# Kernel optimization log

Hardware: AMD Instinct MI355X
Metric: run time of the kernel (lower is better)

## Reference

```python
import jax, jax.numpy as jnp
import numpy as np

SIGMA = 0.02
B, CC, H, W = 4, 21, 96, 96
C_LOW, C_HIGH = 3, 512
N = H * W


def _grid_edges(h, w):
    idx = np.arange(h * w).reshape(h, w)
    eh = np.stack([idx[:, :-1].ravel(), idx[:, 1:].ravel()], 1)
    ev = np.stack([idx[:-1, :].ravel(), idx[1:, :].ravel()], 1)
    return np.concatenate([eh, ev], 0)  # [E,2] 4-connected grid edges


def _mst_bfs(feat, h, w):
    # feat: [C,h,w] numpy. Kruskal MST with norm2 edge weights, then BFS from node 0.
    n = h * w
    edges = _grid_edges(h, w)
    f = feat.reshape(feat.shape[0], -1)
    wts = ((f[:, edges[:, 0]] - f[:, edges[:, 1]]) ** 2).sum(0)
    order = np.argsort(wts, kind='stable')
    uf = np.arange(n)

    def find(x):
        r = x
        while uf[r] != r:
            r = uf[r]
        while uf[x] != r:
            uf[x], x = r, uf[x]
        return r

    adj = [[] for _ in range(n)]
    cnt = 0
    for ei in order:
        a, b = int(edges[ei, 0]), int(edges[ei, 1])
        ra, rb = find(a), find(b)
        if ra != rb:
            uf[ra] = rb
            adj[a].append(b)
            adj[b].append(a)
            cnt += 1
            if cnt == n - 1:
                break
    parent = np.zeros(n, np.int64)
    seen = np.zeros(n, bool)
    seen[0] = True
    levels, frontier = [[0]], [0]
    while frontier:
        nxt = []
        for u in frontier:
            for v in adj[u]:
                if not seen[v]:
                    seen[v] = True
                    parent[v] = u
                    nxt.append(v)
        if nxt:
            levels.append(nxt)
        frontier = nxt
    return parent, levels


def _tree_arrays(embed):
    # Host-side MST + BFS level schedule (integer tree topology, non-differentiable).
    e = np.asarray(jax.device_get(embed)).astype(np.float64)
    bn = e.shape[0]
    parents, levels = [], []
    for b in range(bn):
        p, lv = _mst_bfs(e[b], H, W)
        parents.append(p)
        levels.append(lv)
    D = max(len(lv) for lv in levels)
    L = max(max(len(l) for l in lv) for lv in levels)
    nodes = np.full((bn, D, L), N, np.int32)  # index N = dummy sink node
    for b, lv in enumerate(levels):
        for d, l in enumerate(lv):
            nodes[b, d, :len(l)] = l
    par = np.stack(parents)
    par = np.concatenate([par, np.full((bn, 1), N)], 1).astype(np.int32)
    msk = np.ones((bn, N + 1), np.float32)
    msk[:, 0] = 0.0  # root has no parent edge
    msk[:, N] = 0.0  # dummy node
    return jnp.asarray(nodes), jnp.asarray(par), jnp.asarray(msk)


def _tree_filter(feat, embed, nodes, parent, wmask, sigma):
    # feat [B,C,N], embed [B,Ce,N]. O(N) two-pass (leaf->root, root->leaf) tree DP:
    # out_i = sum_j (prod_{e in path(i,j)} w_e) f_j / same-with-f=1
    bn, c, nn = feat.shape
    ez = jnp.pad(embed, ((0, 0), (0, 0), (0, 1)))  # add dummy column
    ep = jax.vmap(lambda e, p: e[:, p])(ez, parent)  # parent embedding [B,Ce,N+1]
    w = wmask * jnp.exp(-((ez - ep) ** 2).sum(1) / sigma)  # edge weight per node [B,N+1]
    fa = jnp.concatenate([feat, jnp.ones((bn, 1, nn), feat.dtype)], 1)  # append norm channel
    fa = jnp.pad(fa, ((0, 0), (0, 0), (0, 1)))  # [B,C+1,N+1]

    def one(a0, wv, par, lvls):
        def up(a, lvl):  # children before parents: subtree aggregation
            return a.at[:, par[lvl]].add(wv[lvl] * a[:, lvl]), None
        a, _ = jax.lax.scan(up, a0, lvls[::-1])

        def down(s, lvl):  # parents before children: whole-tree aggregation
            wl = wv[lvl]
            sv = a[:, lvl] + wl * (s[:, par[lvl]] - wl * a[:, lvl])
            return s.at[:, lvl].set(sv), None
        s, _ = jax.lax.scan(down, a, lvls)
        return s

    s = jax.vmap(one)(fa, w, parent, nodes)
    return s[:, :c, :nn] / s[:, c:, :nn]


def _nearest(x, h, w):
    hr, wr = x.shape[-2:]
    ri = jnp.arange(h) * hr // h
    ci = jnp.arange(w) * wr // w
    return x[..., ri[:, None], ci[None, :]]


def setup_inputs():
    key = jax.random.key(0)
    k1, k2, k3, k4 = jax.random.split(key, 4)
    preds = jax.random.normal(k1, (B, CC, H, W), jnp.float32)
    low_feats = jax.random.uniform(k2, (B, C_LOW, H, W), dtype=jnp.float32)
    high_feats = 0.03 * jax.random.normal(k3, (B, C_HIGH, H, W), jnp.float32)
    roi = (jax.random.uniform(k4, (B, 1, 2 * H, 2 * W)) > 0.5).astype(jnp.float32)
    return {'preds': preds, 'low_feats': low_feats, 'high_feats': high_feats,
            'unlabeled_ROIs': roi}


def reference(preds, low_feats, high_feats, unlabeled_ROIs):
    nodes_l, par_l, msk_l = _tree_arrays(low_feats)
    nodes_h, par_h, msk_h = _tree_arrays(high_feats)
    roi = _nearest(unlabeled_ROIs, H, W)
    n = roi.sum()
    prob = jax.nn.sigmoid(preds)
    lf = low_feats.reshape(B, C_LOW, N)
    hf = high_feats.reshape(B, C_HIGH, N)
    AS = _tree_filter(prob.reshape(B, CC, N), lf, nodes_l, par_l, msk_l, SIGMA)
    AS = _tree_filter(AS, hf, nodes_h, par_h, msk_h, 1.0)
    loss = (roi * jnp.abs(prob - AS.reshape(B, CC, H, W))).sum()
    return jnp.where(n > 0, loss / n, jnp.zeros_like(loss))
```

## Files before the change

kernel.cpp:

```cpp
#include <hip/hip_runtime.h>
#include <math.h>
#include <stdint.h>
#include <stddef.h>


namespace {
constexpr int Bn  = 4, Cc = 21, Hh = 96, Ww = 96;
constexpr int Nn  = Hh * Ww;
constexpr int EhE = Hh * (Ww - 1);
constexpr int Ne  = EhE + (Hh - 1) * Ww;
constexpr int Clow = 3, Chigh = 512;
constexpr int NCh = Cc + 1;
constexpr int MAXD = 2048;
constexpr int TL  = 2 * (Nn - 1);
constexpr int ESL = 18432;
constexpr int SEG = 19;
constexpr int NR  = (TL + SEG - 1) / SEG;
constexpr int MAXC = 4608;

constexpr size_t OFF_ACC  = 0;
constexpr size_t OFF_PROB = 256;
constexpr size_t OFF_S1   = OFF_PROB + (size_t)Bn * Cc * Nn * 4;
constexpr size_t OFF_S2   = OFF_S1   + (size_t)Bn * NCh * Nn * 4;
constexpr size_t OFF_EW   = OFF_S2   + (size_t)Bn * NCh * Nn * 4;
constexpr size_t OFF_ORD  = OFF_EW   + (size_t)8 * Ne * 8;
constexpr size_t OFF_PPOS = OFF_ORD  + (size_t)8 * Nn * 4;
constexpr size_t OFF_WGT  = OFF_PPOS + (size_t)8 * Nn * 2;
constexpr size_t OFF_LEV  = OFF_WGT  + (size_t)8 * Nn * 4;
constexpr size_t OFF_D    = OFF_LEV  + (size_t)8 * MAXD * 4;
constexpr size_t OFF_DIR  = OFF_D    + 256;
constexpr size_t OFF_CBW  = OFF_DIR  + (size_t)8 * Nn * 4;
constexpr size_t OFF_CBE  = OFF_CBW  + (size_t)8 * Nn * 8;
constexpr size_t OFF_OPP  = OFF_CBE  + (size_t)8 * Nn * 4;
constexpr size_t OFF_SGN  = OFF_OPP  + (size_t)8 * ESL * 2;
constexpr size_t OFF_PNF  = OFF_SGN  + (size_t)8 * ESL;
constexpr size_t OFF_RNK  = OFF_PNF  + (size_t)8 * Nn * 4;
constexpr size_t OFF_PAIR = OFF_RNK  + (size_t)8 * ESL * 2;
constexpr size_t OFF_EL1  = OFF_ORD;
constexpr size_t OFF_EL2  = OFF_WGT;
}

__device__ __forceinline__ void edge_nodes(int e, int& a, int& b) {
    if (e < EhE) { int h = e / (Ww - 1), w = e - h * (Ww - 1); a = h * Ww + w; b = a + 1; }
    else { int e2 = e - EhE; int h = e2 / Ww, w = e2 - h * Ww; a = h * Ww + w; b = a + Ww; }
}
__device__ __forceinline__ int dir_delta(int d) {
    return (d == 0) ? 1 : (d == 1) ? -1 : (d == 2) ? Ww : -Ww;
}
__device__ __forceinline__ int edge_of(int u, int d) {
    int h = u / Ww, w = u - h * Ww;
    if (d == 0) return h * (Ww - 1) + w;
    if (d == 1) return h * (Ww - 1) + w - 1;
    if (d == 2) return EhE + u;
    return EhE + u - Ww;
}

__device__ __forceinline__ unsigned long long mkkey(double w, int e) {
    unsigned long long q = (unsigned long long)(w * 70368744177664.0);
    if (q >= (1ull << 49)) q = (1ull << 49) - 1;
    return (q << 15) | (unsigned)e;
}

__device__ __forceinline__ void compact_push(bool keep, int val, int* cnt,
                                             unsigned short* out, int lane) {
    unsigned long long m = __ballot(keep ? 1 : 0);
    if (m == 0ull) return;
    int leader = __ffsll((unsigned long long)m) - 1;
    int base = 0;
    if (lane == leader) base = atomicAdd(cnt, __popcll(m));
    base = __shfl(base, leader, 64);
    if (keep) {
        unsigned long long lower = m & ((1ull << lane) - 1ull);
        out[base + __popcll(lower)] = (unsigned short)val;
    }
}

__device__ __forceinline__ int scan1024s(int val, int tid, int* wsum) {
    __syncthreads();
    int lane = tid & 63, wv = tid >> 6;
    int x = val;
    #pragma unroll
    for (int off = 1; off < 64; off <<= 1) {
        int y = __shfl_up(x, off, 64);
        if (lane >= off) x += y;
    }
    if (lane == 63) wsum[wv] = x;
    __syncthreads();
    if (wv == 0) {
        int s2 = (lane < 16) ? wsum[lane] : 0;
        #pragma unroll
        for (int off = 1; off < 16; off <<= 1) {
            int y = __shfl_up(s2, off, 64);
            if (lane >= off) s2 += y;
        }
        if (lane < 16) wsum[lane] = s2;
    }
    __syncthreads();
    int base = (wv > 0) ? wsum[wv - 1] : 0;
    return x + base;
}

__device__ __forceinline__ int scan1024_incl(int val, int tid, int* b0, int* b1) {
    b0[tid] = val;
    __syncthreads();
    int* s = b0; int* d = b1;
    for (int off = 1; off < 1024; off <<= 1) {
        int x = s[tid];
        if (tid >= off) x += s[tid - off];
        d[tid] = x;
        __syncthreads();
        int* t = s; s = d; d = t;
    }
    return s[tid];
}

__global__ void k_init(const float* __restrict__ preds, float* __restrict__ prob,
                       double* __restrict__ acc) {
    int idx = blockIdx.x * blockDim.x + threadIdx.x;
    if (idx == 0) { acc[0] = 0.0; acc[1] = 0.0; }
    if (idx >= Bn * Cc * Nn) return;
    prob[idx] = 1.0f / (1.0f + expf(-preds[idx]));
}

__global__ void k_edgew(const float* __restrict__ feat, int C, double* __restrict__ ew) {
    int idx = blockIdx.x * blockDim.x + threadIdx.x;
    if (idx >= Bn * Ne) return;
    int b = idx / Ne, e = idx - b * Ne;
    int a, c2; edge_nodes(e, a, c2);
    const float* fa = feat + (size_t)b * C * Nn + a;
    const float* fb = feat + (size_t)b * C * Nn + c2;
    double s = 0.0;
    int c = 0;
    for (; c + 16 <= C; c += 16) {
        float va[16], vb[16];
        #pragma unroll
        for (int k = 0; k < 16; k++) {
            va[k] = fa[(size_t)(c + k) * Nn];
            vb[k] = fb[(size_t)(c + k) * Nn];
        }
        #pragma unroll
        for (int k = 0; k < 16; k++) {
            double d = (double)va[k] - (double)vb[k];
            s += d * d;
        }
    }
    for (; c < C; c++) {
        double d = (double)fa[(size_t)c * Nn] - (double)fb[(size_t)c * Nn];
        s += d * d;
    }
    ew[idx] = s;
}

__global__ void __launch_bounds__(1024)
k_mst(char* __restrict__ ws) {
    const int tb = blockIdx.x, tid = threadIdx.x;
    const int lane = tid & 63;
    const double* ew = (const double*)(ws + OFF_EW) + (size_t)tb * Ne;
    int* dirG = (int*)(ws + OFF_DIR) + (size_t)tb * Nn;
    unsigned short* elA = (unsigned short*)(ws + OFF_EL1) + (size_t)tb * Ne;
    unsigned short* elB = (unsigned short*)(ws + OFF_EL2) + (size_t)tb * Ne;

    __shared__ unsigned short comp[Nn];
    __shared__ unsigned long long cbK[MAXC];
    __shared__ int scanBuf[2048];
    __shared__ int chgArr[48];
    __shared__ int sLen, sNC;

    unsigned short* nxtN     = (unsigned short*)cbK;
    unsigned short* newSlotN = (unsigned short*)cbK + Nn;
    unsigned short* nxt      = (unsigned short*)cbK;
    unsigned short* newSlot  = (unsigned short*)cbK + MAXC;

    for (int i = tid; i < Nn; i += 1024) dirG[i] = 0;
    if (tid < 48) chgArr[tid] = 0;
    __syncthreads();

    for (int i = tid; i < Nn; i += 1024) {
        int h = i / Ww, w = i - h * Ww;
        unsigned long long bk = ~0ull;
        if (w < Ww - 1) { int e = h * (Ww - 1) + w;     unsigned long long k = mkkey(ew[e], e); if (k < bk) bk = k; }
        if (w > 0)      { int e = h * (Ww - 1) + w - 1; unsigned long long k = mkkey(ew[e], e); if (k < bk) bk = k; }
        if (h < Hh - 1) { int e = EhE + i;              unsigned long long k = mkkey(ew[e], e); if (k < bk) bk = k; }
        if (h > 0)      { int e = EhE + i - Ww;         unsigned long long k = mkkey(ew[e], e); if (k < bk) bk = k; }
        int e = (int)(bk & 0x7FFF);
        int a, c; edge_nodes(e, a, c);
        nxtN[i] = (unsigned short)((a == i) ? c : a);
        int da = (c == a + 1) ? 0 : 2;
        atomicOr(&dirG[a], 1 << da);
        atomicOr(&dirG[c], 1 << (da ^ 1));
    }
    __syncthreads();
    for (int i = tid; i < Nn; i += 1024) {
        int o = nxtN[i];
        if (o != i && nxtN[o] == i && i < o) nxtN[i] = (unsigned short)i;
    }
    __syncthreads();
    {
        int it = 0;
        while (it < 40) {
            bool any = false;
            for (int r = tid; r < Nn; r += 1024) {
                int nr = nxtN[r], nnr = nxtN[nr];
                if (nr != nnr) { nxtN[r] = (unsigned short)nnr; any = true; }
            }
            if (any) chgArr[it] = 1;
            __syncthreads();
            if (!chgArr[it]) break;
            it++;
        }
    }
    {
        int base = tid * 9, cnt = 0, loc[9];
        #pragma unroll
        for (int k = 0; k < 9; k++) {
            int i = base + k;
            loc[k] = cnt;
            if (nxtN[i] == i) cnt++;
        }
        int incl = scan1024_incl(cnt, tid, scanBuf, scanBuf + 1024);
        int eb = incl - cnt;
        #pragma unroll
        for (int k = 0; k < 9; k++) {
            int i = base + k;
            if (nxtN[i] == i) newSlotN[i] = (unsigned short)(eb + loc[k]);
        }
        if (tid == 1023) sNC = incl;
    }
    __syncthreads();
    for (int i = tid; i < Nn; i += 1024) comp[i] = newSlotN[nxtN[i]];
    __syncthreads();
    int nComp = sNC;

    unsigned short* src = elA;
    unsigned short* dst = elB;
    int srcLen = -1;
    for (int round = 2; round < 22 && nComp > 1; round++) {
        if (tid == 0) sLen = 0;
        if (tid < 48) chgArr[tid] = 0;
        __syncthreads();
        if (srcLen < 0) {
            for (int e = tid; e < Ne; e += 1024) {
                int a, c; edge_nodes(e, a, c);
                compact_push(comp[a] != comp[c], e, &sLen, dst, lane);
            }
        } else {
            for (int k = tid; k < srcLen; k += 1024) {
                int e = src[k];
                int a, c; edge_nodes(e, a, c);
                compact_push(comp[a] != comp[c], e, &sLen, dst, lane);
            }
        }
        for (int s = tid; s < nComp; s += 1024) cbK[s] = ~0ull;
        __syncthreads();
        int len = sLen;
        if (len == 0) break;
        for (int k = tid; k < len; k += 1024) {
            int e = dst[k];
            int a, c; edge_nodes(e, a, c);
            unsigned long long key = mkkey(ew[e], e);
            atomicMin(&cbK[comp[a]], key);
            atomicMin(&cbK[comp[c]], key);
        }
        __syncthreads();
        unsigned long long kr[5];
        int nOwn = 0;
        for (int s = tid; s < nComp; s += 1024) kr[nOwn++] = cbK[s];
        __syncthreads();
        {
            int o = 0;
            for (int s = tid; s < nComp; s += 1024, o++) {
                unsigned long long key = kr[o];
                if (key != ~0ull) {
                    int e = (int)(key & 0x7FFF);
                    int a, c; edge_nodes(e, a, c);
                    int sa = comp[a], sc = comp[c];
                    nxt[s] = (unsigned short)((sa == s) ? sc : sa);
                    int da = (c == a + 1) ? 0 : 2;
                    atomicOr(&dirG[a], 1 << da);
                    atomicOr(&dirG[c], 1 << (da ^ 1));
                } else nxt[s] = (unsigned short)s;
            }
        }
        __syncthreads();
        for (int s = tid; s < nComp; s += 1024) {
            int o = nxt[s];
            if (o != s && nxt[o] == s && s < o) nxt[s] = (unsigned short)s;
        }
        __syncthreads();
        {
            int it = 0;
            while (it < 40) {
                bool any = false;
                for (int s = tid; s < nComp; s += 1024) {
                    int ns = nxt[s], nns = nxt[ns];
                    if (ns != nns) { nxt[s] = (unsigned short)nns; any = true; }
                }
                if (any) chgArr[it] = 1;
                __syncthreads();
                if (!chgArr[it]) break;
                it++;
            }
        }
        {
            int K = (nComp + 1023) >> 10;
            int base = tid * K, cnt = 0, loc[5];
            for (int k = 0; k < K; k++) {
                int s = base + k;
                loc[k] = cnt;
                if (s < nComp && nxt[s] == s) cnt++;
            }
            int incl = scan1024_incl(cnt, tid, scanBuf, scanBuf + 1024);
            int eb = incl - cnt;
            for (int k = 0; k < K; k++) {
                int s = base + k;
                if (s < nComp && nxt[s] == s) newSlot[s] = (unsigned short)(eb + loc[k]);
            }
            if (tid == 1023) sNC = incl;
        }
        __syncthreads();
        for (int i = tid; i < Nn; i += 1024) comp[i] = newSlot[nxt[comp[i]]];
        __syncthreads();
        nComp = sNC;
        unsigned short* t = src; src = dst; dst = t;
        srcLen = len;
    }
}

__global__ void __launch_bounds__(1024)
k_topo(char* __restrict__ ws) {
    const int tb = blockIdx.x, tid = threadIdx.x;
    const int lane = tid & 63, wv = tid >> 6;
    const int tree = tb >> 2;
    const double* ew  = (const double*)(ws + OFF_EW) + (size_t)tb * Ne;
    const int*  dirG  = (const int*)(ws + OFF_DIR) + (size_t)tb * Nn;
    unsigned int*   elemSegG = (unsigned int*)(ws + OFF_CBW + (size_t)tb * 73728);
    unsigned short* ORG      = (unsigned short*)(ws + OFF_CBW + (size_t)tb * 73728);
    unsigned short* OWNR     = ORG + ESL;
    unsigned short* ownG     = (unsigned short*)(ws + OFF_CBE + (size_t)tb * (size_t)ESL * 2);
    unsigned short* oppG     = (unsigned short*)(ws + OFF_OPP + (size_t)tb * (size_t)ESL * 2);
    unsigned short* IRG      = (unsigned short*)(ws + OFF_SGN + (size_t)tb * ESL);
    unsigned short* rank0G   = (unsigned short*)(ws + OFF_RNK + (size_t)tb * (size_t)ESL * 2);
    int*            ordG  = (int*)(ws + OFF_ORD)  + (size_t)tb * Nn;
    uint2*          pairG = (uint2*)(ws + OFF_PAIR) + (size_t)tb * Nn;
    int*            levG  = (int*)(ws + OFF_LEV)  + (size_t)tb * MAXD;
    int*            dG    = (int*)(ws + OFF_D);
    const float inv_sigma = tree ? 1.0f : 50.0f;

    __shared__ char A[36864];
    __shared__ char B[18432];
    __shared__ char C[9216];
    __shared__ int  wsum[16];
    __shared__ int  sR, sPack, sCenter;

    unsigned short* degOff = (unsigned short*)B;
    unsigned char*  nbS    = (unsigned char*)C;
    for (int i = tid; i < Nn; i += 1024) nbS[i] = (unsigned char)dirG[i];
    __syncthreads();
    {
        int base9 = tid * 9;
        int loc[9]; int s = 0;
        #pragma unroll
        for (int k = 0; k < 9; k++) { loc[k] = s; s += __popc(nbS[base9 + k]); }
        int incl = scan1024s(s, tid, wsum);
        int eb = incl - s;
        #pragma unroll
        for (int k = 0; k < 9; k++) degOff[base9 + k] = (unsigned short)(eb + loc[k]);
    }
    __syncthreads();

    unsigned short* nxtS = (unsigned short*)A;
    for (int u = tid; u < Nn; u += 1024) {
        int m = nbS[u]; int base = degOff[u]; int k = 0;
        #pragma unroll
        for (int d = 0; d < 4; d++) {
            if (m & (1 << d)) {
                int v = u + dir_delta(d);
                int mv = nbS[v]; int rd = d ^ 1;
                int pv = __popc(mv & ((1 << rd) - 1));
                int dv = __popc(mv);
                int nx = pv + 1; if (nx == dv) nx = 0;
                int j = base + k;
                nxtS[j] = (unsigned short)(degOff[v] + nx);
                ownG[j] = (unsigned short)((u << 2) | d);
                oppG[j] = (unsigned short)(degOff[v] + pv);
                k++;
            }
        }
    }
    __syncthreads();

    int myNr = 0, myLen = 0;
    if (tid < NR) {
        int x = tid * SEG, off = 0;
        for (int g = 0; g < 4096; g++) {
            elemSegG[x] = ((unsigned)tid << 11) | (unsigned)off;
            int y = nxtS[x];
            if (y % SEG == 0) { myNr = y / SEG; myLen = off + 1; break; }
            x = y; off++;
        }
    }
    __syncthreads();

    unsigned short* cn  = (unsigned short*)C;
    unsigned short* cd  = (unsigned short*)(C + 2048);
    unsigned short* nn2 = (unsigned short*)(C + 4096);
    unsigned short* nd2 = (unsigned short*)(C + 6144);
    if (tid == 0)      { cn[0] = 0; cd[0] = 0; }
    else if (tid < NR) { cn[tid] = (unsigned short)myNr; cd[tid] = (unsigned short)myLen; }
    else               { cn[tid] = (unsigned short)tid; cd[tid] = 0; }
    __syncthreads();
    for (int r = 0; r < 10; r++) {
        int c = cn[tid];
        int dv = cd[tid] + cd[c];
        int n2 = cn[c];
        nn2[tid] = (unsigned short)n2; nd2[tid] = (unsigned short)dv;
        __syncthreads();
        unsigned short* t;
        t = cn; cn = nn2; nn2 = t;
        t = cd; cd = nd2; nd2 = t;
    }
    unsigned short* rb = nn2;
    rb[tid] = (tid == 0) ? 0 : (unsigned short)(TL - cd[tid]);
    __syncthreads();

    for (int hh = 0; hh < 2; hh++) {
        unsigned int pk4[9];
        #pragma unroll
        for (int t = 0; t < 9; t++) {
            int e = tid + (hh * 9 + t) * 1024;
            pk4[t] = elemSegG[e < TL ? e : 0];
        }
        unsigned short rbv[9];
        #pragma unroll
        for (int t = 0; t < 9; t++) rbv[t] = rb[pk4[t] >> 11];
        #pragma unroll
        for (int t = 0; t < 9; t++) {
            int e = tid + (hh * 9 + t) * 1024;
            if (e < TL) rank0G[e] = (unsigned short)(rbv[t] + (pk4[t] & 2047));
        }
    }
    __syncthreads();

    for (int hh = 0; hh < 2; hh++) {
        unsigned short rnk[9], opp[9], own2[9];
        #pragma unroll
        for (int t = 0; t < 9; t++) {
            int j = tid + (hh * 9 + t) * 1024;
            int ja = j < TL ? j : 0;
            rnk[t] = rank0G[ja]; opp[t] = oppG[ja]; own2[t] = ownG[ja];
        }
        unsigned short r2[9];
        #pragma unroll
        for (int t = 0; t < 9; t++) r2[t] = rank0G[opp[t]];
        #pragma unroll
        for (int t = 0; t < 9; t++) {
            int j = tid + (hh * 9 + t) * 1024;
            if (j < TL) { int r = rnk[t]; ORG[r] = r2[t]; OWNR[r] = own2[t]; }
        }
    }
    {
        unsigned short dof[9];
        #pragma unroll
        for (int t = 0; t < 9; t++) dof[t] = degOff[tid + t * 1024];
        unsigned short ov[9];
        #pragma unroll
        for (int t = 0; t < 9; t++) ov[t] = oppG[dof[t]];
        unsigned short rv[9];
        #pragma unroll
        for (int t = 0; t < 9; t++) rv[t] = rank0G[ov[t]];
        #pragma unroll
        for (int t = 0; t < 9; t++) IRG[tid + t * 1024] = rv[t];
    }
    __syncthreads();

    short* scanS = (short*)A;
    unsigned char* parC = (unsigned char*)C;
    unsigned short* depthB = (unsigned short*)B;
    int curRoot = 0, rootC = 0;
    for (int ph = 0; ph < 3; ph++) {
        if (tid == 0) {
            sR = ORG[IRG[curRoot]];
            sPack = 0;
        }
        __syncthreads();
        const int R = sR;
        const bool doPar = (ph >= 1);
        int base = tid * 18;
        int n = TL - base; if (n > 18) n = 18; if (n < 0) n = 0;
        unsigned short orvA[18], ownA[18];
        #pragma unroll
        for (int k = 0; k < 18; k++) {
            int q = base + k;
            int r = q + R; if (r >= TL) r -= TL; if (q >= TL) r = 0;
            orvA[k] = ORG[r];
        }
        if (doPar) {
            #pragma unroll
            for (int k = 0; k < 18; k++) {
                int q = base + k;
                int r = q + R; if (r >= TL) r -= TL; if (q >= TL) r = 0;
                ownA[k] = OWNR[r];
            }
        }
        short loc[18]; int s = 0;
        #pragma unroll
        for (int k = 0; k < 18; k++) {
            if (k < n) {
                int q = base + k;
                int rro = (int)orvA[k] - R; if (rro < 0) rro += TL;
                bool desc = q < rro;
                if (doPar && desc) {
                    int own = ownA[k];
                    int head = (own >> 2) + dir_delta(own & 3);
                    parC[head] = (unsigned char)((own & 3) ^ 1);
                }
                s += desc ? 1 : -1;
                loc[k] = (short)s;
            }
        }
        int incl = scan1024s(s, tid, wsum);
        int eb = incl - s;
        #pragma unroll
        for (int k = 0; k < 18; k++)
            if (k < n) scanS[base + k] = (short)(loc[k] + eb);
        __syncthreads();
        int pk = 0;
        {
            unsigned short qA[9];
            #pragma unroll
            for (int j = 0; j < 9; j++) qA[j] = IRG[tid + j * 1024];
            int depA[9];
            #pragma unroll
            for (int j = 0; j < 9; j++) {
                int q = (int)qA[j] - R; if (q < 0) q += TL;
                depA[j] = (int)scanS[q];
            }
            #pragma unroll
            for (int j = 0; j < 9; j++) {
                int x = tid + j * 1024;
                int dep = (x == curRoot) ? 0 : depA[j];
                int p2 = (dep << 14) | x;
                if (p2 > pk) pk = p2;
                if (ph == 2) depthB[x] = (unsigned short)dep;
            }
        }
        #pragma unroll
        for (int off = 32; off > 0; off >>= 1) {
            int o = __shfl_down(pk, off, 64);
            if (o > pk) pk = o;
        }
        if (lane == 0) atomicMax(&sPack, pk);
        __syncthreads();
        if (ph == 0) curRoot = sPack & 16383;
        else if (ph == 1) {
            int diam = sPack >> 14, v = sPack & 16383;
            int steps = diam - (diam >> 1);
            unsigned short* J  = (unsigned short*)A;
            unsigned short* J2 = (unsigned short*)(A + 18432);
            for (int x = tid; x < Nn; x += 1024)
                J[x] = (unsigned short)((x == curRoot) ? x : (x + dir_delta(parC[x])));
            if (tid == 0) sCenter = v;
            __syncthreads();
            for (int k = 0; (steps >> k) != 0; k++) {
                if (tid == 0 && ((steps >> k) & 1)) sCenter = J[sCenter];
                if ((steps >> (k + 1)) != 0) {
                    __syncthreads();
                    for (int x = tid; x < Nn; x += 1024) J2[x] = J[J[x]];
                    __syncthreads();
                    unsigned short* t = J; J = J2; J2 = t;
                }
            }
            __syncthreads();
            curRoot = sCenter;
            rootC = curRoot;
        }
        __syncthreads();
    }
    const int D = (sPack >> 14) + 1;

    unsigned short* posOf = (unsigned short*)A;
    int* hist   = (int*)(A + 18432);
    int* levOff = (int*)(A + 26624);
    for (int k = tid; k < 2048; k += 1024) hist[k] = 0;
    __syncthreads();
    for (int v = tid; v < Nn; v += 1024) atomicAdd(&hist[depthB[v]], 1);
    __syncthreads();
    {
        int h0 = hist[2 * tid], h1 = hist[2 * tid + 1];
        int partial = h0 + h1;
        int incl = scan1024s(partial, tid, wsum);
        int eb = incl - partial;
        levOff[2 * tid] = eb;
        levOff[2 * tid + 1] = eb + h0;
    }
    __syncthreads();
    for (int d = tid; d <= D && d < 2048; d += 1024) levG[d] = levOff[d];
    for (int k = tid; k < 2048; k += 1024) hist[k] = 0;
    __syncthreads();
    for (int v = tid; v < Nn; v += 1024) {
        int dep = depthB[v];
        int pos = levOff[dep] + atomicAdd(&hist[dep], 1);
        posOf[v] = (unsigned short)pos;
        ordG[pos] = v;
    }
    __syncthreads();

    {
        unsigned char rdA[9]; unsigned short posA[9];
        #pragma unroll
        for (int t = 0; t < 9; t++) {
            int v = tid + t * 1024;
            rdA[t] = parC[v]; posA[t] = posOf[v];
        }
        double ewv[9]; unsigned short ppv[9];
        #pragma unroll
        for (int t = 0; t < 9; t++) {
            int v = tid + t * 1024;
            int rd = rdA[t] & 3;
            bool ir = (v == rootC);
            int p  = ir ? v : v + dir_delta(rd);
            int ei = ir ? 0 : edge_of(v, rd);
            ppv[t] = posOf[p];
            ewv[t] = ew[ei];
        }
        #pragma unroll
        for (int t = 0; t < 9; t++) {
            int v = tid + t * 1024;
            int pos = posA[t];
            if (v == rootC) {
                pairG[pos] = make_uint2(0u, 0u);
            } else {
                float w = expf(-(float)ewv[t] * inv_sigma);
                pairG[pos] = make_uint2(__float_as_uint(w), (unsigned)ppv[t]);
            }
        }
    }
    if (tid == 0) dG[tb] = D;
}

__global__ void __launch_bounds__(64)
k_dp(char* __restrict__ ws, int tree, int inMode) {
    const int bc = blockIdx.x;
    const int b = bc / NCh, c = bc % NCh;
    const int tb = tree * Bn + b;
    const int lane = threadIdx.x;
    const int*   ordG  = (const int*)(ws + OFF_ORD)  + (size_t)tb * Nn;
    const uint2* pairG = (const uint2*)(ws + OFF_PAIR) + (size_t)tb * Nn;
    const int*   levG  = (const int*)(ws + OFF_LEV)  + (size_t)tb * MAXD;
    const int D = ((const int*)(ws + OFF_D))[tb];
    const float* src = (inMode == 0)
        ? (const float*)(ws + OFF_PROB) + ((size_t)b * Cc + c) * Nn
        : (const float*)(ws + OFF_S1)   + ((size_t)b * NCh + c) * Nn;
    const float* srcN = (const float*)(ws + OFF_S1) + ((size_t)b * NCh + Cc) * Nn;
    float* dst = (float*)(ws + (tree ? OFF_S2 : OFF_S1)) + ((size_t)b * NCh + c) * Nn;

    __shared__ alignas(16) float Al[Nn];
    __shared__ alignas(16) uint2 pairS[Nn];
    __shared__ unsigned short levS[MAXD];

    {
        const uint4* pg4 = (const uint4*)pairG;
        uint4* ps4 = (uint4*)pairS;
        for (int k = lane; k < Nn / 2; k += 64) ps4[k] = pg4[k];
    }
    for (int d = lane; d <= D && d < MAXD; d += 64) levS[d] = (unsigned short)levG[d];
    if (c == Cc)            { for (int i = lane; i < Nn; i += 64) Al[i] = 1.0f; }
    else if (inMode == 0)   { for (int i = lane; i < Nn; i += 64) Al[i] = src[ordG[i]]; }
    else                    { for (int i = lane; i < Nn; i += 64) { int nd = ordG[i]; Al[i] = src[nd] / srcN[nd]; } }
    __builtin_amdgcn_wave_barrier();
    asm volatile("" ::: "memory");

    if (D > 1) {
        int sd = levS[D - 1], sd1 = levS[D];
        for (int d = D - 1; d >= 1; d--) {
            int nbv = (d > 1) ? (int)levS[d - 1] : 0;
            for (int i = sd + lane; i < sd1; i += 64) {
                uint2 pk = pairS[i];
                atomicAdd(&Al[pk.y], __uint_as_float(pk.x) * Al[i]);
            }
            __builtin_amdgcn_wave_barrier();
            asm volatile("" ::: "memory");
            sd1 = sd; sd = nbv;
        }
    }
    if (D > 1) {
        int sd = levS[1], sd1 = levS[2];
        for (int d = 1; d < D; d++) {
            int nbv = (d + 2 <= D) ? (int)levS[d + 2] : 0;
            for (int i = sd + lane; i < sd1; i += 64) {
                uint2 pk = pairS[i];
                float w = __uint_as_float(pk.x);
                float a = Al[i];
                Al[i] = a + w * (Al[pk.y] - w * a);
            }
            __builtin_amdgcn_wave_barrier();
            asm volatile("" ::: "memory");
            sd = sd1; sd1 = nbv;
        }
    }
    __builtin_amdgcn_wave_barrier();
    asm volatile("" ::: "memory");
    for (int i = lane; i < Nn; i += 64) dst[ordG[i]] = Al[i];
}

__global__ void k_loss(char* __restrict__ ws, const float* __restrict__ roi) {
    const int tid = threadIdx.x;
    int idx = blockIdx.x * 256 + tid;
    const float* prob = (const float*)(ws + OFF_PROB);
    const float* S2   = (const float*)(ws + OFF_S2);
    double* acc = (double*)(ws + OFF_ACC);
    double ls = 0.0, cnt = 0.0;
    if (idx < Bn * Cc * Nn) {
        int b = idx / (Cc * Nn);
        int rem = idx - b * (Cc * Nn);
        int c = rem / Nn, n = rem - c * Nn;
        int h = n / Ww, w2 = n - h * Ww;
        float r = roi[(size_t)b * (2 * Hh) * (2 * Ww) + (size_t)(2 * h) * (2 * Ww) + 2 * w2];
        float as = S2[((size_t)b * NCh + c) * Nn + n] / S2[((size_t)b * NCh + Cc) * Nn + n];
        float pp = prob[((size_t)b * Cc + c) * Nn + n];
        ls = (double)(r * fabsf(pp - as));
        if (c == 0) cnt = (double)r;
    }
    __shared__ double sl[256], sc2[256];
    sl[tid] = ls; sc2[tid] = cnt;
    __syncthreads();
    for (int s = 128; s > 0; s >>= 1) {
        if (tid < s) { sl[tid] += sl[tid + s]; sc2[tid] += sc2[tid + s]; }
        __syncthreads();
    }
    if (tid == 0) { atomicAdd(acc, sl[0]); atomicAdd(acc + 1, sc2[0]); }
}

__global__ void k_final(const double* __restrict__ acc, float* __restrict__ out) {
    if (blockIdx.x == 0 && threadIdx.x == 0)
        out[0] = (acc[1] > 0.0) ? (float)(acc[0] / acc[1]) : 0.0f;
}

extern "C" void kernel_launch(void* const* d_in, const int* in_sizes, int n_in,
                              void* d_out, int out_size, void* d_ws, size_t ws_size,
                              hipStream_t stream) {
    const float* preds = (const float*)d_in[0];
    const float* lowf  = (const float*)d_in[1];
    const float* highf = (const float*)d_in[2];
    const float* roi   = (const float*)d_in[3];
    char* ws = (char*)d_ws;
    float* out = (float*)d_out;
    double* ewl = (double*)(ws + OFF_EW);
    double* ewh = (double*)(ws + OFF_EW) + (size_t)Bn * Ne;

    k_init<<<(Bn * Cc * Nn + 255) / 256, 256, 0, stream>>>(
        preds, (float*)(ws + OFF_PROB), (double*)(ws + OFF_ACC));
    k_edgew<<<(Bn * Ne + 255) / 256, 256, 0, stream>>>(lowf, Clow, ewl);
    k_edgew<<<(Bn * Ne + 255) / 256, 256, 0, stream>>>(highf, Chigh, ewh);
    k_mst<<<8, 1024, 0, stream>>>(ws);
    k_topo<<<8, 1024, 0, stream>>>(ws);
    k_dp<<<Bn * NCh, 64, 0, stream>>>(ws, 0, 0);
    k_dp<<<Bn * NCh, 64, 0, stream>>>(ws, 1, 1);
    k_loss<<<(Bn * Cc * Nn + 255) / 256, 256, 0, stream>>>(ws, roi);
    k_final<<<1, 64, 0, stream>>>((const double*)(ws + OFF_ACC), out);
}
```

Baseline: 676.7 us.

## Replace upward-pass LDS atomic scatter with child-mask gather in tree DP

After: 898.3 us. 32.8% more time.

```diff
diff --git a/kernel.cpp b/kernel.cpp
--- a/kernel.cpp
+++ b/kernel.cpp
@@ -36,6 +36,7 @@
 constexpr size_t OFF_PNF  = OFF_SGN  + (size_t)8 * ESL;
 constexpr size_t OFF_RNK  = OFF_PNF  + (size_t)8 * Nn * 4;
 constexpr size_t OFF_PAIR = OFF_RNK  + (size_t)8 * ESL * 2;
+constexpr size_t OFF_POSF = OFF_PAIR + (size_t)8 * Nn * 8;
 constexpr size_t OFF_EL1  = OFF_ORD;
 constexpr size_t OFF_EL2  = OFF_WGT;
 }
@@ -342,6 +343,7 @@
     unsigned short* rank0G   = (unsigned short*)(ws + OFF_RNK + (size_t)tb * (size_t)ESL * 2);
     int*            ordG  = (int*)(ws + OFF_ORD)  + (size_t)tb * Nn;
     uint2*          pairG = (uint2*)(ws + OFF_PAIR) + (size_t)tb * Nn;
+    unsigned short* posOfG = (unsigned short*)(ws + OFF_POSF) + (size_t)tb * Nn;
     int*            levG  = (int*)(ws + OFF_LEV)  + (size_t)tb * MAXD;
     int*            dG    = (int*)(ws + OFF_D);
     const float inv_sigma = tree ? 1.0f : 50.0f;
@@ -606,11 +608,22 @@
     __syncthreads();
 
     {
-        unsigned char rdA[9]; unsigned short posA[9];
+        unsigned char rdA[9]; unsigned short posA[9]; int mkA[9];
         #pragma unroll
         for (int t = 0; t < 9; t++) {
             int v = tid + t * 1024;
             rdA[t] = parC[v]; posA[t] = posOf[v];
+        }
+        #pragma unroll
+        for (int t = 0; t < 9; t++) {
+            int v = tid + t * 1024;
+            int h = v / Ww, w2 = v - h * Ww;
+            int mk = 0;
+            if (w2 < Ww - 1) { int u = v + 1;  if (u != rootC && parC[u] == 1) mk |= 1; }
+            if (w2 > 0)      { int u = v - 1;  if (u != rootC && parC[u] == 0) mk |= 2; }
+            if (h < Hh - 1)  { int u = v + Ww; if (u != rootC && parC[u] == 3) mk |= 4; }
+            if (h > 0)       { int u = v - Ww; if (u != rootC && parC[u] == 2) mk |= 8; }
+            mkA[t] = mk;
         }
         double ewv[9]; unsigned short ppv[9];
         #pragma unroll
@@ -627,11 +640,13 @@
         for (int t = 0; t < 9; t++) {
             int v = tid + t * 1024;
             int pos = posA[t];
+            posOfG[v] = (unsigned short)pos;
+            unsigned meta = ((unsigned)mkA[t] << 14) | ((unsigned)v << 18);
             if (v == rootC) {
-                pairG[pos] = make_uint2(0u, 0u);
+                pairG[pos] = make_uint2(0u, meta);
             } else {
                 float w = expf(-(float)ewv[t] * inv_sigma);
-                pairG[pos] = make_uint2(__float_as_uint(w), (unsigned)ppv[t]);
+                pairG[pos] = make_uint2(__float_as_uint(w), (unsigned)ppv[t] | meta);
             }
         }
     }
@@ -646,6 +661,7 @@
     const int lane = threadIdx.x;
     const int*   ordG  = (const int*)(ws + OFF_ORD)  + (size_t)tb * Nn;
     const uint2* pairG = (const uint2*)(ws + OFF_PAIR) + (size_t)tb * Nn;
+    const unsigned short* posOfG = (const unsigned short*)(ws + OFF_POSF) + (size_t)tb * Nn;
     const int*   levG  = (const int*)(ws + OFF_LEV)  + (size_t)tb * MAXD;
     const int D = ((const int*)(ws + OFF_D))[tb];
     const float* src = (inMode == 0)
@@ -656,12 +672,16 @@
 
     __shared__ alignas(16) float Al[Nn];
     __shared__ alignas(16) uint2 pairS[Nn];
+    __shared__ alignas(16) unsigned short posOfS[Nn];
     __shared__ unsigned short levS[MAXD];
 
     {
         const uint4* pg4 = (const uint4*)pairG;
         uint4* ps4 = (uint4*)pairS;
         for (int k = lane; k < Nn / 2; k += 64) ps4[k] = pg4[k];
+        const uint4* po4 = (const uint4*)posOfG;
+        uint4* pos4 = (uint4*)posOfS;
+        for (int k = lane; k < Nn / 8; k += 64) pos4[k] = po4[k];
     }
     for (int d = lane; d <= D && d < MAXD; d += 64) levS[d] = (unsigned short)levG[d];
     if (c == Cc)            { for (int i = lane; i < Nn; i += 64) Al[i] = 1.0f; }
@@ -670,13 +690,24 @@
     __builtin_amdgcn_wave_barrier();
     asm volatile("" ::: "memory");
 
-    if (D > 1) {
+    {
         int sd = levS[D - 1], sd1 = levS[D];
-        for (int d = D - 1; d >= 1; d--) {
-            int nbv = (d > 1) ? (int)levS[d - 1] : 0;
+        for (int d = D - 1; d >= 0; d--) {
+            int nbv = (d > 0) ? (int)levS[d - 1] : 0;
             for (int i = sd + lane; i < sd1; i += 64) {
                 uint2 pk = pairS[i];
-                atomicAdd(&Al[pk.y], __uint_as_float(pk.x) * Al[i]);
+                int v = (int)(pk.y >> 18);
+                unsigned mk = (pk.y >> 14) & 0xFu;
+                float a = Al[i];
+                if (mk & 1u) { int cp = posOfS[v + 1];
+                    a = __fadd_rn(a, __fmul_rn(__uint_as_float(pairS[cp].x), Al[cp])); }
+                if (mk & 2u) { int cp = posOfS[v - 1];
+                    a = __fadd_rn(a, __fmul_rn(__uint_as_float(pairS[cp].x), Al[cp])); }
+                if (mk & 4u) { int cp = posOfS[v + Ww];
+                    a = __fadd_rn(a, __fmul_rn(__uint_as_float(pairS[cp].x), Al[cp])); }
+                if (mk & 8u) { int cp = posOfS[v - Ww];
+                    a = __fadd_rn(a, __fmul_rn(__uint_as_float(pairS[cp].x), Al[cp])); }
+                Al[i] = a;
             }
             __builtin_amdgcn_wave_barrier();
             asm volatile("" ::: "memory");
@@ -691,7 +722,7 @@
                 uint2 pk = pairS[i];
                 float w = __uint_as_float(pk.x);
                 float a = Al[i];
-                Al[i] = a + w * (Al[pk.y] - w * a);
+                Al[i] = a + w * (Al[(int)(pk.y & 0x3FFFu)] - w * a);
             }
             __builtin_amdgcn_wave_barrier();
             asm volatile("" ::: "memory");
```

## Process top-down tree pass three levels per step using precomputed ancestors

Applied to the files above, without the earlier changes.

After: 713.7 us. +5.5%, slower.

```diff
diff --git a/kernel.cpp b/kernel.cpp
--- a/kernel.cpp
+++ b/kernel.cpp
@@ -36,6 +36,7 @@
 constexpr size_t OFF_PNF  = OFF_SGN  + (size_t)8 * ESL;
 constexpr size_t OFF_RNK  = OFF_PNF  + (size_t)8 * Nn * 4;
 constexpr size_t OFF_PAIR = OFF_RNK  + (size_t)8 * ESL * 2;
+constexpr size_t OFF_ANC3 = OFF_PAIR + (size_t)8 * Nn * 8;
 constexpr size_t OFF_EL1  = OFF_ORD;
 constexpr size_t OFF_EL2  = OFF_WGT;
 }
@@ -342,6 +343,7 @@
     unsigned short* rank0G   = (unsigned short*)(ws + OFF_RNK + (size_t)tb * (size_t)ESL * 2);
     int*            ordG  = (int*)(ws + OFF_ORD)  + (size_t)tb * Nn;
     uint2*          pairG = (uint2*)(ws + OFF_PAIR) + (size_t)tb * Nn;
+    unsigned short* anc3G = (unsigned short*)(ws + OFF_ANC3) + (size_t)tb * Nn;
     int*            levG  = (int*)(ws + OFF_LEV)  + (size_t)tb * MAXD;
     int*            dG    = (int*)(ws + OFF_D);
     const float inv_sigma = tree ? 1.0f : 50.0f;
@@ -612,26 +614,51 @@
             int v = tid + t * 1024;
             rdA[t] = parC[v]; posA[t] = posOf[v];
         }
-        double ewv[9]; unsigned short ppv[9];
+        int p1A[9];
         #pragma unroll
         for (int t = 0; t < 9; t++) {
             int v = tid + t * 1024;
-            int rd = rdA[t] & 3;
-            bool ir = (v == rootC);
-            int p  = ir ? v : v + dir_delta(rd);
-            int ei = ir ? 0 : edge_of(v, rd);
-            ppv[t] = posOf[p];
+            p1A[t] = (v == rootC) ? v : v + dir_delta(rdA[t] & 3);
+        }
+        unsigned char rd1A[9];
+        #pragma unroll
+        for (int t = 0; t < 9; t++) rd1A[t] = parC[p1A[t]];
+        int p2A[9];
+        #pragma unroll
+        for (int t = 0; t < 9; t++)
+            p2A[t] = (p1A[t] == rootC) ? p1A[t] : p1A[t] + dir_delta(rd1A[t] & 3);
+        unsigned char rd2A[9];
+        #pragma unroll
+        for (int t = 0; t < 9; t++) rd2A[t] = parC[p2A[t]];
+        int p3A[9];
+        #pragma unroll
+        for (int t = 0; t < 9; t++)
+            p3A[t] = (p2A[t] == rootC) ? p2A[t] : p2A[t] + dir_delta(rd2A[t] & 3);
+        unsigned short pp1[9], pp2[9], pp3[9];
+        #pragma unroll
+        for (int t = 0; t < 9; t++) {
+            pp1[t] = posOf[p1A[t]];
+            pp2[t] = posOf[p2A[t]];
+            pp3[t] = posOf[p3A[t]];
+        }
+        double ewv[9];
+        #pragma unroll
+        for (int t = 0; t < 9; t++) {
+            int v = tid + t * 1024;
+            int ei = (v == rootC) ? 0 : edge_of(v, rdA[t] & 3);
             ewv[t] = ew[ei];
         }
         #pragma unroll
         for (int t = 0; t < 9; t++) {
             int v = tid + t * 1024;
             int pos = posA[t];
+            anc3G[pos] = pp3[t];
             if (v == rootC) {
                 pairG[pos] = make_uint2(0u, 0u);
             } else {
                 float w = expf(-(float)ewv[t] * inv_sigma);
-                pairG[pos] = make_uint2(__float_as_uint(w), (unsigned)ppv[t]);
+                pairG[pos] = make_uint2(__float_as_uint(w),
+                                        (unsigned)pp1[t] | ((unsigned)pp2[t] << 14));
             }
         }
     }
@@ -646,6 +673,7 @@
     const int lane = threadIdx.x;
     const int*   ordG  = (const int*)(ws + OFF_ORD)  + (size_t)tb * Nn;
     const uint2* pairG = (const uint2*)(ws + OFF_PAIR) + (size_t)tb * Nn;
+    const unsigned short* anc3G = (const unsigned short*)(ws + OFF_ANC3) + (size_t)tb * Nn;
     const int*   levG  = (const int*)(ws + OFF_LEV)  + (size_t)tb * MAXD;
     const int D = ((const int*)(ws + OFF_D))[tb];
     const float* src = (inMode == 0)
@@ -656,12 +684,16 @@
 
     __shared__ alignas(16) float Al[Nn];
     __shared__ alignas(16) uint2 pairS[Nn];
+    __shared__ alignas(16) unsigned short anc3S[Nn];
     __shared__ unsigned short levS[MAXD];
 
     {
         const uint4* pg4 = (const uint4*)pairG;
         uint4* ps4 = (uint4*)pairS;
         for (int k = lane; k < Nn / 2; k += 64) ps4[k] = pg4[k];
+        const uint4* a34 = (const uint4*)anc3G;
+        uint4* as4 = (uint4*)anc3S;
+        for (int k = lane; k < Nn / 8; k += 64) as4[k] = a34[k];
     }
     for (int d = lane; d <= D && d < MAXD; d += 64) levS[d] = (unsigned short)levG[d];
     if (c == Cc)            { for (int i = lane; i < Nn; i += 64) Al[i] = 1.0f; }
@@ -676,7 +708,7 @@
             int nbv = (d > 1) ? (int)levS[d - 1] : 0;
             for (int i = sd + lane; i < sd1; i += 64) {
                 uint2 pk = pairS[i];
-                atomicAdd(&Al[pk.y], __uint_as_float(pk.x) * Al[i]);
+                atomicAdd(&Al[pk.y & 0x3FFFu], __uint_as_float(pk.x) * Al[i]);
             }
             __builtin_amdgcn_wave_barrier();
             asm volatile("" ::: "memory");
@@ -684,18 +716,41 @@
         }
     }
     if (D > 1) {
-        int sd = levS[1], sd1 = levS[2];
-        for (int d = 1; d < D; d++) {
-            int nbv = (d + 2 <= D) ? (int)levS[d + 2] : 0;
-            for (int i = sd + lane; i < sd1; i += 64) {
-                uint2 pk = pairS[i];
-                float w = __uint_as_float(pk.x);
-                float a = Al[i];
-                Al[i] = a + w * (Al[pk.y] - w * a);
-            }
-            __builtin_amdgcn_wave_barrier();
-            asm volatile("" ::: "memory");
-            sd = sd1; sd1 = nbv;
+        for (int d0 = 1; d0 < D; d0 += 3) {
+            int dEnd = d0 + 3 < D ? d0 + 3 : D;
+            int bS = levS[d0], bE = levS[dEnd];
+            int L1 = levS[d0 + 1 < D ? d0 + 1 : D];
+            int L2 = levS[d0 + 2 < D ? d0 + 2 : D];
+            int nch = (bE - bS + 63) >> 6;
+            for (int ch = nch - 1; ch >= 0; --ch) {
+                int i = bS + ch * 64 + lane;
+                if (i < bE) {
+                    uint2 pk = pairS[i];
+                    float w = __uint_as_float(pk.x);
+                    int pp = (int)(pk.y & 0x3FFFu);
+                    int a2 = (int)((pk.y >> 14) & 0x3FFFu);
+                    int j = (i >= L1) + (i >= L2);
+                    float sAb;
+                    if (j == 0) {
+                        sAb = Al[pp];
+                    } else if (j == 1) {
+                        float up = Al[pp], sa2 = Al[a2];
+                        float wp = __uint_as_float(pairS[pp].x);
+                        sAb = up + wp * (sa2 - wp * up);
+                    } else {
+                        int a3 = (int)anc3S[i];
+                        float up = Al[pp], ua2 = Al[a2], sa3 = Al[a3];
+                        float wp  = __uint_as_float(pairS[pp].x);
+                        float wa2 = __uint_as_float(pairS[a2].x);
+                        float s2 = ua2 + wa2 * (sa3 - wa2 * ua2);
+                        sAb = up + wp * (s2 - wp * up);
+                    }
+                    float a = Al[i];
+                    Al[i] = a + w * (sAb - w * a);
+                }
+                __builtin_amdgcn_wave_barrier();
+                asm volatile("" ::: "memory");
+            }
         }
     }
     __builtin_amdgcn_wave_barrier();
```
